# Kernel optimization log

Hardware: AMD Instinct MI355X
Metric: run time of the kernel (lower is better)

Reference implementation:

```python
import jax, jax.numpy as jnp
import numpy as np

B = 8192          # number of parallel trajectories
L = 64            # controller hidden width
MAX_STEPS = 500   # fixed unroll cap for the data-dependent while loop
GOAL_P = 0.5
MIN_P = -1.2
MIN_V, MAX_V = -0.07, 0.07
MIN_ACC, MAX_ACC = -1.2, 1.2


def setup_inputs() -> dict:
    key = jax.random.key(0)
    k0, k1, k2 = jax.random.split(key, 3)
    # initial state: p ~ U[-0.6,-0.4], v = u = reward = 0  -> [B, 4]
    p0 = jax.random.uniform(k0, (B,), minval=-0.6, maxval=-0.4)
    z = jnp.zeros((B,), jnp.float32)
    x = jnp.stack([p0, z, z, z], axis=1)
    w1 = jax.random.normal(k1, (2, L), jnp.float32) / np.float32(np.sqrt(2.0))
    b1 = jnp.zeros((L,), jnp.float32)
    w2 = jax.random.normal(k2, (L, 1), jnp.float32) / np.float32(np.sqrt(L))
    b2 = jnp.zeros((1,), jnp.float32)
    return {"x": x, "w1": w1, "b1": b1, "w2": w2, "b2": b2}


def reference(x, w1, b1, w2, b2):
    def step(state, _):
        p, v, u, r = state[:, 0], state[:, 1], state[:, 2], state[:, 3]
        active = p <= GOAL_P                      # while1 test on x[0]
        # ifelse_p: if p <= min_position -> p=-1.2, v=0
        hit = p <= MIN_P
        p1 = jnp.where(hit, MIN_P, p)
        v1 = jnp.where(hit, 0.0, v)
        # assign_acceleration: u = tanh(W2 relu(W1 [p,v] + b1) + b2)
        h = jax.nn.relu(jnp.stack([p1, v1], axis=1) @ w1 + b1)   # [B, L]
        u1 = jnp.tanh(h @ w2 + b2)[:, 0]                         # [B]
        # ifelse_acceleration: clamp u to [min_acc, max_acc]
        u1 = jnp.clip(u1, MIN_ACC, MAX_ACC)
        # assign_reward_update: r = r + u*u*(-0.1)
        r1 = r - 0.1 * u1 * u1
        # assign_v: v = v + 0.0015*u - 0.0025*cos(3p), then clamp (ifelse_v)
        v2 = jnp.clip(v1 + 0.0015 * u1 - 0.0025 * jnp.cos(3.0 * p1), MIN_V, MAX_V)
        # assign_update_p: p = p + v
        p2 = p1 + v2
        new = jnp.stack([p2, v2, u1, r1], axis=1)
        state = jnp.where(active[:, None], new, state)           # freeze finished trajectories
        return state, None

    state, _ = jax.lax.scan(step, x, None, length=MAX_STEPS)
    # check_position: if p <= goal -> skip, else reward += 100
    p = state[:, 0]
    r = jnp.where(p <= GOAL_P, state[:, 3], state[:, 3] + 100.0)
    return state.at[:, 3].set(r)
```

## Files before the change

### kernel.cpp

```cpp
#include <hip/hip_runtime.h>


constexpr int B = 8192;
constexpr int L = 64;
constexpr int MAX_STEPS = 500;
constexpr float GOAL_P = 0.5f;
constexpr float MIN_P  = -1.2f;
constexpr float MIN_V  = -0.07f;
constexpr float MAX_V  = 0.07f;

constexpr int KL  = 16;
constexpr int UPL = L / KL;

template<int CTRL>
__device__ __forceinline__ float dpp_add(float x) {
  int y = __builtin_amdgcn_update_dpp(0, __float_as_int(x), CTRL, 0xf, 0xf, true);
  return x + __int_as_float(y);
}

__global__ __launch_bounds__(256) void mc_kernel(
    const float* __restrict__ x,  const float* __restrict__ w1,
    const float* __restrict__ b1, const float* __restrict__ w2,
    const float* __restrict__ b2, float* __restrict__ out)
{
  int tid = blockIdx.x * blockDim.x + threadIdx.x;
  int env = tid >> 4;
  int sub = tid & 15;

  constexpr float TS = 2.8853900817779268f;

  float w1a[UPL], w1b[UPL], b1r[UPL], w2r[UPL];
  const int j0 = sub * UPL;
#pragma unroll
  for (int i = 0; i < UPL; ++i) {
    w1a[i] = w1[j0 + i];
    w1b[i] = w1[L + j0 + i];
    b1r[i] = b1[j0 + i];
    w2r[i] = w2[j0 + i] * TS;
  }
  const float b2v = b2[0] * TS;

  float4 st = reinterpret_cast<const float4*>(x)[env];
  float p = st.x, v = st.y, u = st.z, r = st.w;

  for (int stp = 0; stp < MAX_STEPS; ++stp) {
    bool active = (p <= GOAL_P);
    if (!__any(active)) break;

    float p1 = fmaxf(p, MIN_P);
    float v1 = (p <= MIN_P) ? 0.0f : v;

    float h0 = fmaxf(fmaf(v1, w1b[0], fmaf(p1, w1a[0], b1r[0])), 0.0f);
    float h1 = fmaxf(fmaf(v1, w1b[1], fmaf(p1, w1a[1], b1r[1])), 0.0f);
    float h2 = fmaxf(fmaf(v1, w1b[2], fmaf(p1, w1a[2], b1r[2])), 0.0f);
    float h3 = fmaxf(fmaf(v1, w1b[3], fmaf(p1, w1a[3], b1r[3])), 0.0f);
    float s0 = fmaf(h2, w2r[2], h0 * w2r[0]);
    float s1 = fmaf(h3, w2r[3], h1 * w2r[1]);
    float s  = s0 + s1;

    s = dpp_add<0xB1>(s);
    s = dpp_add<0x4E>(s);
    s = dpp_add<0x141>(s);
    s = dpp_add<0x140>(s);

    float a  = fabsf(s + b2v);
    float e  = __builtin_amdgcn_exp2f(a);
    float t  = fmaf(-2.0f, __builtin_amdgcn_rcpf(e + 1.0f), 1.0f);
    float u1 = copysignf(t, s + b2v);

    float r1 = fmaf(-0.1f * u1, u1, r);

    float c = __builtin_amdgcn_cosf(p1 * 0.47746482927568601f);

    float v2 = fmaf(-0.0025f, c, fmaf(0.0015f, u1, v1));
    v2 = fminf(fmaxf(v2, MIN_V), MAX_V);
    float p2 = p1 + v2;

    if (active) { p = p2; v = v2; u = u1; r = r1; }
  }

  if (sub == 0) {
    float rout = (p <= GOAL_P) ? r : r + 100.0f;
    reinterpret_cast<float4*>(out)[env] = make_float4(p, v, u, rout);
  }
}

extern "C" void kernel_launch(void* const* d_in, const int* in_sizes, int n_in,
                              void* d_out, int out_size, void* d_ws, size_t ws_size,
                              hipStream_t stream) {
  const float* x  = (const float*)d_in[0];
  const float* w1 = (const float*)d_in[1];
  const float* b1 = (const float*)d_in[2];
  const float* w2 = (const float*)d_in[3];
  const float* b2 = (const float*)d_in[4];
  float* out = (float*)d_out;

  constexpr int threads = B * KL;
  mc_kernel<<<threads / 256, 256, 0, stream>>>(x, w1, b1, w2, b2, out);
}
```

Measured before the change: 92.68 us.

## Process two trajectories per thread with packed float2 math and early per-env writeback

Each 16-lane group now handles two environments using 2-wide vector math, which can map to packed FP32 instructions, and halves the thread count. The tanh is simplified by dropping the abs/copysign, and b2 is folded into the reduction seed. Finished trajectories are detected with ballots and written out immediately instead of carrying a per-step active select. Reward is accumulated as a sum of u^2. The intent is more ILP and fewer instructions per step, at the cost of half as many waves and a tanh form that relies on exp2 not overflowing.

```diff
diff --git a/kernel.cpp b/kernel.cpp
--- a/kernel.cpp
+++ b/kernel.cpp
@@ -1,5 +1,7 @@
 #include <hip/hip_runtime.h>
 
+
+typedef float v2f __attribute__((ext_vector_type(2)));
 
 constexpr int B = 8192;
 constexpr int L = 64;
@@ -11,77 +13,118 @@
 
 constexpr int KL  = 16;
 constexpr int UPL = L / KL;
+constexpr int EPT = 2;
 
 template<int CTRL>
-__device__ __forceinline__ float dpp_add(float x) {
-  int y = __builtin_amdgcn_update_dpp(0, __float_as_int(x), CTRL, 0xf, 0xf, true);
-  return x + __int_as_float(y);
+__device__ __forceinline__ v2f dpp_add2(v2f x) {
+  int yx = __builtin_amdgcn_update_dpp(0, __float_as_int(x.x), CTRL, 0xf, 0xf, true);
+  int yy = __builtin_amdgcn_update_dpp(0, __float_as_int(x.y), CTRL, 0xf, 0xf, true);
+  return x + (v2f){__int_as_float(yx), __int_as_float(yy)};
 }
 
-__global__ __launch_bounds__(256) void mc_kernel(
+__global__ __launch_bounds__(256, 1) void mc_kernel(
     const float* __restrict__ x,  const float* __restrict__ w1,
     const float* __restrict__ b1, const float* __restrict__ w2,
     const float* __restrict__ b2, float* __restrict__ out)
 {
-  int tid = blockIdx.x * blockDim.x + threadIdx.x;
-  int env = tid >> 4;
-  int sub = tid & 15;
+  int tid  = blockIdx.x * blockDim.x + threadIdx.x;
+  int grp  = tid >> 4;
+  int sub  = tid & 15;
+  int lane = threadIdx.x & 63;
 
   constexpr float TS = 2.8853900817779268f;
 
-  float w1a[UPL], w1b[UPL], b1r[UPL], w2r[UPL];
+  v2f W1A[UPL], W1B[UPL], B1R[UPL], W2R[UPL];
   const int j0 = sub * UPL;
 #pragma unroll
   for (int i = 0; i < UPL; ++i) {
-    w1a[i] = w1[j0 + i];
-    w1b[i] = w1[L + j0 + i];
-    b1r[i] = b1[j0 + i];
-    w2r[i] = w2[j0 + i] * TS;
+    float a = w1[j0 + i], b = w1[L + j0 + i], c = b1[j0 + i],
+          d = w2[j0 + i] * TS;
+    W1A[i] = (v2f){a, a};
+    W1B[i] = (v2f){b, b};
+    B1R[i] = (v2f){c, c};
+    W2R[i] = (v2f){d, d};
   }
-  const float b2v = b2[0] * TS;
+  const float bseed = (sub == 0) ? b2[0] * TS : 0.0f;
+  const v2f sv0 = {bseed, bseed};
 
-  float4 st = reinterpret_cast<const float4*>(x)[env];
-  float p = st.x, v = st.y, u = st.z, r = st.w;
+  float4 st0 = reinterpret_cast<const float4*>(x)[grp * EPT + 0];
+  float4 st1 = reinterpret_cast<const float4*>(x)[grp * EPT + 1];
+  v2f p = {st0.x, st1.x}, v = {st0.y, st1.y}, u = {st0.z, st1.z};
+  const v2f r0 = {st0.w, st1.w};
+  v2f racc = {0.0f, 0.0f};
+
+  unsigned long long live0 = __ballot(true);
+  unsigned long long live1 = live0;
 
   for (int stp = 0; stp < MAX_STEPS; ++stp) {
-    bool active = (p <= GOAL_P);
-    if (!__any(active)) break;
+    v2f p1 = __builtin_elementwise_max(p, (v2f){MIN_P, MIN_P});
+    v2f v1 = { (p.x <= MIN_P) ? 0.0f : v.x,
+               (p.y <= MIN_P) ? 0.0f : v.y };
 
-    float p1 = fmaxf(p, MIN_P);
-    float v1 = (p <= MIN_P) ? 0.0f : v;
+    float c0 = __builtin_amdgcn_cosf(p1.x * 0.47746482927568601f);
+    float c1 = __builtin_amdgcn_cosf(p1.y * 0.47746482927568601f);
 
-    float h0 = fmaxf(fmaf(v1, w1b[0], fmaf(p1, w1a[0], b1r[0])), 0.0f);
-    float h1 = fmaxf(fmaf(v1, w1b[1], fmaf(p1, w1a[1], b1r[1])), 0.0f);
-    float h2 = fmaxf(fmaf(v1, w1b[2], fmaf(p1, w1a[2], b1r[2])), 0.0f);
-    float h3 = fmaxf(fmaf(v1, w1b[3], fmaf(p1, w1a[3], b1r[3])), 0.0f);
-    float s0 = fmaf(h2, w2r[2], h0 * w2r[0]);
-    float s1 = fmaf(h3, w2r[3], h1 * w2r[1]);
-    float s  = s0 + s1;
+    v2f s = sv0;
+#pragma unroll
+    for (int i = 0; i < UPL; ++i) {
+      v2f h = __builtin_elementwise_fma(v1, W1B[i],
+              __builtin_elementwise_fma(p1, W1A[i], B1R[i]));
+      h = __builtin_elementwise_max(h, (v2f){0.0f, 0.0f});
+      s = __builtin_elementwise_fma(h, W2R[i], s);
+    }
 
-    s = dpp_add<0xB1>(s);
-    s = dpp_add<0x4E>(s);
-    s = dpp_add<0x141>(s);
-    s = dpp_add<0x140>(s);
+    s = dpp_add2<0xB1>(s);
+    s = dpp_add2<0x4E>(s);
+    s = dpp_add2<0x141>(s);
+    s = dpp_add2<0x140>(s);
 
-    float a  = fabsf(s + b2v);
-    float e  = __builtin_amdgcn_exp2f(a);
-    float t  = fmaf(-2.0f, __builtin_amdgcn_rcpf(e + 1.0f), 1.0f);
-    float u1 = copysignf(t, s + b2v);
+    float e0 = __builtin_amdgcn_exp2f(s.x);
+    float e1 = __builtin_amdgcn_exp2f(s.y);
+    float q0 = __builtin_amdgcn_rcpf(e0 + 1.0f);
+    float q1 = __builtin_amdgcn_rcpf(e1 + 1.0f);
+    v2f u1 = { fmaf(-2.0f, q0, 1.0f), fmaf(-2.0f, q1, 1.0f) };
 
-    float r1 = fmaf(-0.1f * u1, u1, r);
+    v2f vc = __builtin_elementwise_fma((v2f){-0.0025f, -0.0025f}, (v2f){c0, c1},
+             __builtin_elementwise_fma((v2f){0.0015f, 0.0015f}, u1, v1));
+    v2f v2c = { __builtin_amdgcn_fmed3f(vc.x, MIN_V, MAX_V),
+                __builtin_amdgcn_fmed3f(vc.y, MIN_V, MAX_V) };
 
-    float c = __builtin_amdgcn_cosf(p1 * 0.47746482927568601f);
+    p = p1 + v2c;
+    v = v2c;
+    u = u1;
+    racc = __builtin_elementwise_fma(u1, u1, racc);
 
-    float v2 = fmaf(-0.0025f, c, fmaf(0.0015f, u1, v1));
-    v2 = fminf(fmaxf(v2, MIN_V), MAX_V);
-    float p2 = p1 + v2;
-
-    if (active) { p = p2; v = v2; u = u1; r = r1; }
+    unsigned long long c0m = __ballot(p.x > GOAL_P) & live0;
+    unsigned long long c1m = __ballot(p.y > GOAL_P) & live1;
+    if (c0m | c1m) {
+      live0 &= ~c0m;
+      live1 &= ~c1m;
+      if (((c0m >> lane) & 1ull) && sub == 0) {
+        float rout = fmaf(-0.1f, racc.x, r0.x) + 100.0f;
+        reinterpret_cast<float4*>(out)[grp * EPT + 0] =
+            make_float4(p.x, v.x, u.x, rout);
+      }
+      if (((c1m >> lane) & 1ull) && sub == 0) {
+        float rout = fmaf(-0.1f, racc.y, r0.y) + 100.0f;
+        reinterpret_cast<float4*>(out)[grp * EPT + 1] =
+            make_float4(p.y, v.y, u.y, rout);
+      }
+      if (!(live0 | live1)) return;
+    }
   }
 
   if (sub == 0) {
-    float rout = (p <= GOAL_P) ? r : r + 100.0f;
-    reinterpret_cast<float4*>(out)[env] = make_float4(p, v, u, rout);
+    if ((live0 >> lane) & 1ull) {
+      float rout = fmaf(-0.1f, racc.x, r0.x);
+      reinterpret_cast<float4*>(out)[grp * EPT + 0] =
+          make_float4(p.x, v.x, u.x, rout);
+    }
+    if ((live1 >> lane) & 1ull) {
+      float rout = fmaf(-0.1f, racc.y, r0.y);
+      reinterpret_cast<float4*>(out)[grp * EPT + 1] =
+          make_float4(p.y, v.y, u.y, rout);
+    }
   }
 }
 
@@ -95,6 +138,6 @@
   const float* b2 = (const float*)d_in[4];
   float* out = (float*)d_out;
 
-  constexpr int threads = B * KL;
+  constexpr int threads = (B / EPT) * KL;
   mc_kernel<<<threads / 256, 256, 0, stream>>>(x, w1, b1, w2, b2, out);
 }
```

After: 123.8 us. +33.5%, slower.
